# Kernel optimization log

Measured on AMD Instinct MI355X. Metric: run time of the kernel, lower is better.

## Reference

```python
import jax, jax.numpy as jnp
import numpy as np

# KernelRnn.slow_update for one converted parameter, time_lag_covariance=None path:
#   var <- variance_update / time_index - mean_update**2
#   update = concat([mean_update, var], axis=0)            # [2R, m, n]
#   val = Q @ update (contract rule axis)                  # [C,  m, n]
#   new_chemical = y*chemical + z*(tanh(K_slow @ chemical) + val)
#   h = v @ new_chemical                                   # [m, n]

C = 5       # numberOfSlowChemicals
R = 14      # numberUpdateRules (all rules enabled)
M, N = 2048, 1024  # underlying weight matrix shape


def setup_inputs() -> dict:
    key = jax.random.key(0)
    ks = jax.random.split(key, 8)
    chemical = jax.random.normal(ks[0], (C, M, N), dtype=jnp.float32)
    mean_update = jax.random.normal(ks[1], (R, M, N), dtype=jnp.float32)
    variance_update = jax.random.uniform(ks[2], (R, M, N), dtype=jnp.float32)
    Q = jax.random.normal(ks[3], (C, 2 * R), dtype=jnp.float32) * 0.01
    K_slow = jax.random.normal(ks[4], (C, C), dtype=jnp.float32) * 0.01
    v = jnp.ones((1, C), dtype=jnp.float32) / C
    # tau-spaced decay vectors as in init_slow_params
    min_tau, max_tau = 2.0, 50.0
    tau = min_tau * (max_tau / min_tau) ** jnp.linspace(0.0, 1.0, C)
    z = (1.0 / tau).astype(jnp.float32)
    y = (1.0 - z).astype(jnp.float32)
    return {
        "chemical": chemical,
        "mean_update": mean_update,
        "variance_update": variance_update,
        "Q": Q,
        "K_slow": K_slow,
        "v": v,
        "y": y,
        "z": z,
        "time_index": 10,
    }


def reference(chemical, mean_update, variance_update, Q, K_slow, v, y, z, time_index):
    inv_t = 1.0 / jnp.asarray(time_index, dtype=chemical.dtype)
    var = variance_update * inv_t - mean_update * mean_update        # [R, m, n]
    update = jnp.concatenate([mean_update, var], axis=0)             # [2R, m, n]
    val = jnp.einsum('cr,rmn->cmn', Q, update)                       # [C, m, n]
    mixed = jnp.tanh(jnp.einsum('cd,dmn->cmn', K_slow, chemical))    # [C, m, n]
    new_chemical = (y[:, None, None] * chemical
                    + z[:, None, None] * (mixed + val))              # [C, m, n]
    h = jnp.einsum('oc,cmn->omn', v, new_chemical)[0]                # [m, n]
    return h
```

## Files before the change

### kernel.cpp

```cpp
#include <hip/hip_runtime.h>


#define CC 5
#define RR 14
#define VU 2

typedef float f32x4 __attribute__((ext_vector_type(4)));

__global__ void prep_kernel(const float* __restrict__ Q,
                            const float* __restrict__ Ks,
                            const float* __restrict__ v,
                            const float* __restrict__ y,
                            const float* __restrict__ z,
                            const int* __restrict__ tindex,
                            float* __restrict__ cf) {
    int i = threadIdx.x;
    float inv_t = 1.0f / (float)tindex[0];
    if (i < RR) {
        float a = 0.0f, b = 0.0f;
        #pragma unroll
        for (int c = 0; c < CC; ++c) {
            float vz = v[c] * z[c];
            a = fmaf(vz, Q[c * (2 * RR) + i], a);
            b = fmaf(vz, Q[c * (2 * RR) + RR + i], b);
        }
        cf[i] = a;
        cf[16 + i] = b * inv_t;
        cf[32 + i] = b;
    } else if (i < RR + CC) {
        int c = i - RR;
        cf[48 + c] = v[c] * y[c];
        cf[53 + c] = v[c] * z[c];
    } else if (i < RR + CC + CC * CC) {
        int j = i - (RR + CC);
        cf[58 + j] = Ks[j];
    }
}

__device__ __forceinline__ float fast_tanh(float x) {
    float e = __expf(2.0f * x);
    return fmaf(-2.0f, __builtin_amdgcn_rcpf(e + 1.0f), 1.0f);
}

__global__ __launch_bounds__(256)
void fused_kernel(const float* __restrict__ chem,
                  const float* __restrict__ meanu,
                  const float* __restrict__ varu,
                  const float* __restrict__ cf,
                  float* __restrict__ out,
                  int P) {
    const int tid = threadIdx.x;
    const size_t tile = (size_t)blockIdx.x * (256 * VU * 4);

    f32x4 acc[VU];
    #pragma unroll
    for (int u = 0; u < VU; ++u) acc[u] = (f32x4)(0.f);

    #pragma unroll 1
    for (int r = 0; r < RR; ++r) {
        const f32x4* pm = reinterpret_cast<const f32x4*>(meanu + (size_t)r * P + tile);
        const f32x4* pv = reinterpret_cast<const f32x4*>(varu  + (size_t)r * P + tile);
        f32x4 m[VU], w[VU];
        #pragma unroll
        for (int u = 0; u < VU; ++u) m[u] = __builtin_nontemporal_load(pm + u * 256 + tid);
        #pragma unroll
        for (int u = 0; u < VU; ++u) w[u] = __builtin_nontemporal_load(pv + u * 256 + tid);
        float ar = cf[r], bir = cf[16 + r], br = cf[32 + r];
        #pragma unroll
        for (int u = 0; u < VU; ++u) {
            acc[u].x = fmaf(ar, m[u].x, acc[u].x);
            acc[u].y = fmaf(ar, m[u].y, acc[u].y);
            acc[u].z = fmaf(ar, m[u].z, acc[u].z);
            acc[u].w = fmaf(ar, m[u].w, acc[u].w);
            acc[u].x = fmaf(bir, w[u].x, acc[u].x);
            acc[u].y = fmaf(bir, w[u].y, acc[u].y);
            acc[u].z = fmaf(bir, w[u].z, acc[u].z);
            acc[u].w = fmaf(bir, w[u].w, acc[u].w);
            acc[u].x = fmaf(-br, m[u].x * m[u].x, acc[u].x);
            acc[u].y = fmaf(-br, m[u].y * m[u].y, acc[u].y);
            acc[u].z = fmaf(-br, m[u].z * m[u].z, acc[u].z);
            acc[u].w = fmaf(-br, m[u].w * m[u].w, acc[u].w);
        }
    }

    f32x4 ch[CC][VU];
    #pragma unroll
    for (int c = 0; c < CC; ++c) {
        const f32x4* pc = reinterpret_cast<const f32x4*>(chem + (size_t)c * P + tile);
        #pragma unroll
        for (int u = 0; u < VU; ++u) ch[c][u] = __builtin_nontemporal_load(pc + u * 256 + tid);
    }

    #pragma unroll
    for (int u = 0; u < VU; ++u) {
        #pragma unroll
        for (int c = 0; c < CC; ++c) {
            float vy = cf[48 + c];
            acc[u].x = fmaf(vy, ch[c][u].x, acc[u].x);
            acc[u].y = fmaf(vy, ch[c][u].y, acc[u].y);
            acc[u].z = fmaf(vy, ch[c][u].z, acc[u].z);
            acc[u].w = fmaf(vy, ch[c][u].w, acc[u].w);
        }
        #pragma unroll
        for (int c = 0; c < CC; ++c) {
            f32x4 s = (f32x4)(0.f);
            #pragma unroll
            for (int d = 0; d < CC; ++d) {
                float k = cf[58 + c * CC + d];
                s.x = fmaf(k, ch[d][u].x, s.x);
                s.y = fmaf(k, ch[d][u].y, s.y);
                s.z = fmaf(k, ch[d][u].z, s.z);
                s.w = fmaf(k, ch[d][u].w, s.w);
            }
            float vz = cf[53 + c];
            acc[u].x = fmaf(vz, fast_tanh(s.x), acc[u].x);
            acc[u].y = fmaf(vz, fast_tanh(s.y), acc[u].y);
            acc[u].z = fmaf(vz, fast_tanh(s.z), acc[u].z);
            acc[u].w = fmaf(vz, fast_tanh(s.w), acc[u].w);
        }
    }

    f32x4* po = reinterpret_cast<f32x4*>(out + tile);
    #pragma unroll
    for (int u = 0; u < VU; ++u) po[u * 256 + tid] = acc[u];
}

extern "C" void kernel_launch(void* const* d_in, const int* in_sizes, int n_in,
                              void* d_out, int out_size, void* d_ws, size_t ws_size,
                              hipStream_t stream) {
    const float* chem  = (const float*)d_in[0];
    const float* meanu = (const float*)d_in[1];
    const float* varu  = (const float*)d_in[2];
    const float* Q     = (const float*)d_in[3];
    const float* Ks    = (const float*)d_in[4];
    const float* v     = (const float*)d_in[5];
    const float* y     = (const float*)d_in[6];
    const float* z     = (const float*)d_in[7];
    const int*   ti    = (const int*)d_in[8];

    float* cf = (float*)d_ws;
    float* out = (float*)d_out;

    prep_kernel<<<1, 64, 0, stream>>>(Q, Ks, v, y, z, ti, cf);

    int P = out_size;
    int tile_elems = 256 * VU * 4;
    int blocks = (P + tile_elems - 1) / tile_elems;
    fused_kernel<<<blocks, 256, 0, stream>>>(chem, meanu, varu, cf, out, P);
}
```

Baseline: 262.0 us.

## Fold coefficient prep into main kernel and unroll rule loop by two

Removes the separate single-block prep kernel. Each block now computes the folded coefficients into shared memory before a barrier, which saves one launch and the global round trip. The rule loop handles two rules per iteration so more loads are in flight, and output stores become nontemporal. In exchange every block redundantly recomputes the tiny coefficient table and pays a __syncthreads.

```diff
diff --git a/kernel.cpp b/kernel.cpp
--- a/kernel.cpp
+++ b/kernel.cpp
@@ -7,49 +7,55 @@
 
 typedef float f32x4 __attribute__((ext_vector_type(4)));
 
-__global__ void prep_kernel(const float* __restrict__ Q,
-                            const float* __restrict__ Ks,
-                            const float* __restrict__ v,
-                            const float* __restrict__ y,
-                            const float* __restrict__ z,
-                            const int* __restrict__ tindex,
-                            float* __restrict__ cf) {
-    int i = threadIdx.x;
-    float inv_t = 1.0f / (float)tindex[0];
-    if (i < RR) {
-        float a = 0.0f, b = 0.0f;
-        #pragma unroll
-        for (int c = 0; c < CC; ++c) {
-            float vz = v[c] * z[c];
-            a = fmaf(vz, Q[c * (2 * RR) + i], a);
-            b = fmaf(vz, Q[c * (2 * RR) + RR + i], b);
-        }
-        cf[i] = a;
-        cf[16 + i] = b * inv_t;
-        cf[32 + i] = b;
-    } else if (i < RR + CC) {
-        int c = i - RR;
-        cf[48 + c] = v[c] * y[c];
-        cf[53 + c] = v[c] * z[c];
-    } else if (i < RR + CC + CC * CC) {
-        int j = i - (RR + CC);
-        cf[58 + j] = Ks[j];
-    }
-}
-
 __device__ __forceinline__ float fast_tanh(float x) {
     float e = __expf(2.0f * x);
     return fmaf(-2.0f, __builtin_amdgcn_rcpf(e + 1.0f), 1.0f);
+}
+
+__device__ __forceinline__ void fma4(f32x4& acc, float s, const f32x4& x) {
+    acc.x = fmaf(s, x.x, acc.x);
+    acc.y = fmaf(s, x.y, acc.y);
+    acc.z = fmaf(s, x.z, acc.z);
+    acc.w = fmaf(s, x.w, acc.w);
 }
 
 __global__ __launch_bounds__(256)
 void fused_kernel(const float* __restrict__ chem,
                   const float* __restrict__ meanu,
                   const float* __restrict__ varu,
-                  const float* __restrict__ cf,
+                  const float* __restrict__ Q,
+                  const float* __restrict__ Ks,
+                  const float* __restrict__ vv,
+                  const float* __restrict__ yy,
+                  const float* __restrict__ zz,
+                  const int* __restrict__ tindex,
                   float* __restrict__ out,
                   int P) {
+    __shared__ float cf[96];
     const int tid = threadIdx.x;
+
+    if (tid < RR) {
+        float inv_t = 1.0f / (float)tindex[0];
+        float a = 0.0f, b = 0.0f;
+        #pragma unroll
+        for (int c = 0; c < CC; ++c) {
+            float vz = vv[c] * zz[c];
+            a = fmaf(vz, Q[c * (2 * RR) + tid], a);
+            b = fmaf(vz, Q[c * (2 * RR) + RR + tid], b);
+        }
+        cf[tid] = a;
+        cf[16 + tid] = b * inv_t;
+        cf[32 + tid] = b;
+    } else if (tid < RR + CC) {
+        int c = tid - RR;
+        cf[48 + c] = vv[c] * yy[c];
+        cf[53 + c] = vv[c] * zz[c];
+    } else if (tid < RR + CC + CC * CC) {
+        int j = tid - (RR + CC);
+        cf[58 + j] = Ks[j];
+    }
+    __syncthreads();
+
     const size_t tile = (size_t)blockIdx.x * (256 * VU * 4);
 
     f32x4 acc[VU];
@@ -57,29 +63,31 @@
     for (int u = 0; u < VU; ++u) acc[u] = (f32x4)(0.f);
 
     #pragma unroll 1
-    for (int r = 0; r < RR; ++r) {
-        const f32x4* pm = reinterpret_cast<const f32x4*>(meanu + (size_t)r * P + tile);
-        const f32x4* pv = reinterpret_cast<const f32x4*>(varu  + (size_t)r * P + tile);
-        f32x4 m[VU], w[VU];
-        #pragma unroll
-        for (int u = 0; u < VU; ++u) m[u] = __builtin_nontemporal_load(pm + u * 256 + tid);
-        #pragma unroll
-        for (int u = 0; u < VU; ++u) w[u] = __builtin_nontemporal_load(pv + u * 256 + tid);
-        float ar = cf[r], bir = cf[16 + r], br = cf[32 + r];
+    for (int r = 0; r < RR; r += 2) {
+        const f32x4* pm0 = reinterpret_cast<const f32x4*>(meanu + (size_t)r * P + tile);
+        const f32x4* pv0 = reinterpret_cast<const f32x4*>(varu  + (size_t)r * P + tile);
+        const f32x4* pm1 = reinterpret_cast<const f32x4*>(meanu + (size_t)(r + 1) * P + tile);
+        const f32x4* pv1 = reinterpret_cast<const f32x4*>(varu  + (size_t)(r + 1) * P + tile);
+        f32x4 m0[VU], w0[VU], m1[VU], w1[VU];
         #pragma unroll
         for (int u = 0; u < VU; ++u) {
-            acc[u].x = fmaf(ar, m[u].x, acc[u].x);
-            acc[u].y = fmaf(ar, m[u].y, acc[u].y);
-            acc[u].z = fmaf(ar, m[u].z, acc[u].z);
-            acc[u].w = fmaf(ar, m[u].w, acc[u].w);
-            acc[u].x = fmaf(bir, w[u].x, acc[u].x);
-            acc[u].y = fmaf(bir, w[u].y, acc[u].y);
-            acc[u].z = fmaf(bir, w[u].z, acc[u].z);
-            acc[u].w = fmaf(bir, w[u].w, acc[u].w);
-            acc[u].x = fmaf(-br, m[u].x * m[u].x, acc[u].x);
-            acc[u].y = fmaf(-br, m[u].y * m[u].y, acc[u].y);
-            acc[u].z = fmaf(-br, m[u].z * m[u].z, acc[u].z);
-            acc[u].w = fmaf(-br, m[u].w * m[u].w, acc[u].w);
+            m0[u] = __builtin_nontemporal_load(pm0 + u * 256 + tid);
+            w0[u] = __builtin_nontemporal_load(pv0 + u * 256 + tid);
+            m1[u] = __builtin_nontemporal_load(pm1 + u * 256 + tid);
+            w1[u] = __builtin_nontemporal_load(pv1 + u * 256 + tid);
+        }
+        float a0 = cf[r],     bi0 = cf[16 + r],     b0 = cf[32 + r];
+        float a1 = cf[r + 1], bi1 = cf[16 + r + 1], b1 = cf[32 + r + 1];
+        #pragma unroll
+        for (int u = 0; u < VU; ++u) {
+            fma4(acc[u], a0, m0[u]);
+            fma4(acc[u], bi0, w0[u]);
+            f32x4 mm0 = m0[u] * m0[u];
+            fma4(acc[u], -b0, mm0);
+            fma4(acc[u], a1, m1[u]);
+            fma4(acc[u], bi1, w1[u]);
+            f32x4 mm1 = m1[u] * m1[u];
+            fma4(acc[u], -b1, mm1);
         }
     }
 
@@ -95,22 +103,14 @@
     for (int u = 0; u < VU; ++u) {
         #pragma unroll
         for (int c = 0; c < CC; ++c) {
-            float vy = cf[48 + c];
-            acc[u].x = fmaf(vy, ch[c][u].x, acc[u].x);
-            acc[u].y = fmaf(vy, ch[c][u].y, acc[u].y);
-            acc[u].z = fmaf(vy, ch[c][u].z, acc[u].z);
-            acc[u].w = fmaf(vy, ch[c][u].w, acc[u].w);
+            fma4(acc[u], cf[48 + c], ch[c][u]);
         }
         #pragma unroll
         for (int c = 0; c < CC; ++c) {
             f32x4 s = (f32x4)(0.f);
             #pragma unroll
             for (int d = 0; d < CC; ++d) {
-                float k = cf[58 + c * CC + d];
-                s.x = fmaf(k, ch[d][u].x, s.x);
-                s.y = fmaf(k, ch[d][u].y, s.y);
-                s.z = fmaf(k, ch[d][u].z, s.z);
-                s.w = fmaf(k, ch[d][u].w, s.w);
+                fma4(s, cf[58 + c * CC + d], ch[d][u]);
             }
             float vz = cf[53 + c];
             acc[u].x = fmaf(vz, fast_tanh(s.x), acc[u].x);
@@ -122,7 +122,8 @@
 
     f32x4* po = reinterpret_cast<f32x4*>(out + tile);
     #pragma unroll
-    for (int u = 0; u < VU; ++u) po[u * 256 + tid] = acc[u];
+    for (int u = 0; u < VU; ++u)
+        __builtin_nontemporal_store(acc[u], po + u * 256 + tid);
 }
 
 extern "C" void kernel_launch(void* const* d_in, const int* in_sizes, int n_in,
@@ -138,13 +139,11 @@
     const float* z     = (const float*)d_in[7];
     const int*   ti    = (const int*)d_in[8];
 
-    float* cf = (float*)d_ws;
     float* out = (float*)d_out;
-
-    prep_kernel<<<1, 64, 0, stream>>>(Q, Ks, v, y, z, ti, cf);
+    (void)d_ws; (void)ws_size;
 
     int P = out_size;
     int tile_elems = 256 * VU * 4;
     int blocks = (P + tile_elems - 1) / tile_elems;
-    fused_kernel<<<blocks, 256, 0, stream>>>(chem, meanu, varu, cf, out, P);
+    fused_kernel<<<blocks, 256, 0, stream>>>(chem, meanu, varu, Q, Ks, v, y, z, ti, out, P);
 }
```

Measured after the change: 263.7 us. No clear change (+0.7%).
